# Performance work log

Measured on AMD Instinct MI355X. Metric: run time of the kernel, lower is better.

Reference implementation:

```python
import jax, jax.numpy as jnp
import numpy as np

B, S, H, NH, HD = 2, 2048, 1024, 16, 64
THETA = 10000.0


def setup_inputs() -> dict:
    key = jax.random.key(0)
    k1, k2, k3, k4, k5 = jax.random.split(key, 5)
    hidden_states = jax.random.normal(k1, (B, S, H), dtype=jnp.float32)
    # RoPE tables, interleaved-pair layout: [c0,c0,c1,c1,...] along head_dim
    inv_freq = 1.0 / (THETA ** (jnp.arange(0, HD, 2, dtype=jnp.float32) / HD))
    t = jnp.arange(S, dtype=jnp.float32)
    freqs = jnp.outer(t, inv_freq)                      # [S, HD//2]
    freqs_cos = jnp.repeat(jnp.cos(freqs), 2, axis=-1)  # [S, HD]
    freqs_sin = jnp.repeat(jnp.sin(freqs), 2, axis=-1)  # [S, HD]
    position_ids = jnp.arange(S, dtype=jnp.int32)
    w = 0.02
    Wq = jax.random.normal(k2, (H, H), dtype=jnp.float32) * w
    Wk = jax.random.normal(k3, (H, H), dtype=jnp.float32) * w
    Wv = jax.random.normal(k4, (H, H), dtype=jnp.float32) * w
    Wo = jax.random.normal(k5, (H, H), dtype=jnp.float32) * w
    return {"hidden_states": hidden_states, "freqs_cos": freqs_cos,
            "freqs_sin": freqs_sin, "position_ids": position_ids,
            "Wq": Wq, "Wk": Wk, "Wv": Wv, "Wo": Wo}


def _rotate_half_interleaved(x):
    # stack([-x[..., 1::2], x[..., ::2]], -1).reshape_as(x)
    xe = x.reshape(x.shape[:-1] + (HD // 2, 2))
    return jnp.stack([-xe[..., 1], xe[..., 0]], axis=-1).reshape(x.shape)


def reference(hidden_states, freqs_cos, freqs_sin, position_ids, Wq, Wk, Wv, Wo):
    b, s, _ = hidden_states.shape
    # QKV projections (torch Linear: y = x @ W.T), split into heads [b, nh, s, hd]
    q = jnp.einsum('bsh,oh->bso', hidden_states, Wq).reshape(b, s, NH, HD).transpose(0, 2, 1, 3)
    k = jnp.einsum('bsh,oh->bso', hidden_states, Wk).reshape(b, s, NH, HD).transpose(0, 2, 1, 3)
    v = jnp.einsum('bsh,oh->bso', hidden_states, Wv).reshape(b, s, NH, HD).transpose(0, 2, 1, 3)
    cos = freqs_cos[position_ids][None, None]  # [1, 1, s, hd]
    sin = freqs_sin[position_ids][None, None]
    rq = _rotate_half_interleaved(q)
    # NOTE: faithful to source bug — rotate_half_k is built from q, not k
    q = q * cos + rq * sin
    k = k * cos + rq * sin
    # causal SDPA, scale = 1/sqrt(head_dim)
    scores = jnp.einsum('bhqd,bhkd->bhqk', q, k) / jnp.sqrt(jnp.float32(HD))
    causal = jnp.tril(jnp.ones((s, s), dtype=bool))
    scores = jnp.where(causal, scores, jnp.float32(-1e30))
    attn = jax.nn.softmax(scores, axis=-1)
    out = jnp.einsum('bhqk,bhkd->bhqd', attn, v)
    out = out.transpose(0, 2, 1, 3).reshape(b, s, H)
    return jnp.einsum('bsh,oh->bso', out, Wo)
```

## Files before the change

kernel.cpp:

```cpp
#include <hip/hip_runtime.h>
#include <stdint.h>

#define BB 2
#define SS 2048
#define HH 1024
#define NHH 16
#define HDD 64

typedef short bf16s;
typedef __attribute__((ext_vector_type(8))) short short8;
typedef __attribute__((ext_vector_type(4))) short short4v;
typedef __attribute__((ext_vector_type(2))) short short2v;
typedef __attribute__((ext_vector_type(4))) float f32x4;
typedef _Float16 half4v __attribute__((ext_vector_type(4)));
typedef _Float16 half8v __attribute__((ext_vector_type(8)));
typedef __fp16 fp16x2 __attribute__((ext_vector_type(2)));

__device__ inline short f2bf(float f) {
  union { float f; uint32_t u; } v; v.f = f;
  uint32_t r = (v.u + 0x7fffu + ((v.u >> 16) & 1u)) >> 16;
  return (short)r;
}
__device__ inline float bf2f(short h) {
  union { uint32_t u; float f; } v; v.u = ((uint32_t)(uint16_t)h) << 16;
  return v.f;
}

__device__ __forceinline__ float exp2_raw(float x) {
  float r;
  asm("v_exp_f32 %0, %1\n\ts_nop 0" : "=v"(r) : "v"(x));
  return r;
}

__device__ inline void gld_lds16(const void* g, void* l) {
  __builtin_amdgcn_global_load_lds((const __attribute__((address_space(1))) void*)g,
                                   (__attribute__((address_space(3))) void*)l, 16, 0, 0);
}

__device__ inline void stv(short* C, size_t i, float v) { C[i] = f2bf(v); }
__device__ inline void stv(float* C, size_t i, float v) { C[i] = v; }

__device__ inline f32x4 mfma_k32(short8 a, short8 b, f32x4 c) {
  return __builtin_amdgcn_mfma_f32_16x16x32_bf16(a, b, c, 0, 0, 0);
}
__device__ inline f32x4 mfma_k32(half8v a, half8v b, f32x4 c) {
  return __builtin_amdgcn_mfma_f32_16x16x32_f16(a, b, c, 0, 0, 0);
}
template <typename ET> struct ftr;
template <> struct ftr<short>     { using v8 = short8; };
template <> struct ftr<_Float16>  { using v8 = half8v; };

__global__ __launch_bounds__(256) void convert_all(
    const float* __restrict__ x, const float* __restrict__ Wq,
    const float* __restrict__ Wk, const float* __restrict__ Wv,
    const float* __restrict__ Wo, bf16s* __restrict__ xb,
    bf16s* __restrict__ wqkv, _Float16* __restrict__ wof) {
  const long M1 = 1024L * 1024L;
  long e = (long)(blockIdx.x * blockDim.x + threadIdx.x) * 4;
  if (e < 7 * M1) {
    const float* src; bf16s* dst;
    if (e < 4 * M1)      { src = x  + e;            dst = xb   + e; }
    else if (e < 5 * M1) { src = Wq + (e - 4 * M1); dst = wqkv + (e - 4 * M1); }
    else if (e < 6 * M1) { src = Wk + (e - 5 * M1); dst = wqkv + (e - 4 * M1); }
    else                 { src = Wv + (e - 6 * M1); dst = wqkv + (e - 4 * M1); }
    float4 v = *(const float4*)src;
    short4v o;
    o.x = f2bf(v.x); o.y = f2bf(v.y); o.z = f2bf(v.z); o.w = f2bf(v.w);
    *(short4v*)dst = o;
  } else {
    float4 v = *(const float4*)(Wo + (e - 7 * M1));
    half4v o;
    o.x = (_Float16)v.x; o.y = (_Float16)v.y;
    o.z = (_Float16)v.z; o.w = (_Float16)v.w;
    *(half4v*)(wof + (e - 7 * M1)) = o;
  }
}

template <typename ET, typename OT, int MT>
__global__ __launch_bounds__(256) void gemm_bt(
    const ET* __restrict__ A, const ET* __restrict__ Bm,
    OT* __restrict__ C, int K, int ldc) {
  using V8 = typename ftr<ET>::v8;
  __shared__ __align__(16) ET As[MT * 32 * 64];
  __shared__ __align__(16) ET Bs[128 * 64];
  const int tid = threadIdx.x;
  const int lane = tid & 63, w = tid >> 6;
  const int quad = lane >> 4, mcol = lane & 15;
  const int bm = blockIdx.y * (MT * 32), bn = blockIdx.x * 128;
  const int wm = (w >> 1) * (MT * 16), wn = (w & 1) * 64;
  f32x4 acc[MT][4] = {};
  const int nkt = K >> 6;
  for (int kt = 0; kt < nkt; ++kt) {
    __syncthreads();
#pragma unroll
    for (int i = 0; i < MT; ++i) {
      int seg = (i * 4 + w) * 512;
      int flat = seg + lane * 8;
      int row = flat >> 6;
      int cpos = (flat >> 3) & 7;
      int cs = cpos ^ (row & 7);
      gld_lds16(A + (size_t)(bm + row) * K + kt * 64 + cs * 8, &As[seg]);
    }
#pragma unroll
    for (int i = 0; i < 4; ++i) {
      int seg = (i * 4 + w) * 512;
      int flat = seg + lane * 8;
      int row = flat >> 6;
      int cpos = (flat >> 3) & 7;
      int cs = cpos ^ (row & 7);
      gld_lds16(Bm + (size_t)(bn + row) * K + kt * 64 + cs * 8, &Bs[seg]);
    }
    __syncthreads();
#pragma unroll
    for (int ks = 0; ks < 2; ++ks) {
      V8 af[MT], bf[4];
#pragma unroll
      for (int mt = 0; mt < MT; ++mt) {
        int row = wm + mt * 16 + mcol;
        int cs = (ks * 4 + quad) ^ (row & 7);
        af[mt] = *(const V8*)&As[row * 64 + cs * 8];
      }
#pragma unroll
      for (int nt = 0; nt < 4; ++nt) {
        int row = wn + nt * 16 + mcol;
        int cs = (ks * 4 + quad) ^ (row & 7);
        bf[nt] = *(const V8*)&Bs[row * 64 + cs * 8];
      }
#pragma unroll
      for (int mt = 0; mt < MT; ++mt)
#pragma unroll
        for (int nt = 0; nt < 4; ++nt)
          acc[mt][nt] = mfma_k32(af[mt], bf[nt], acc[mt][nt]);
    }
  }
#pragma unroll
  for (int mt = 0; mt < MT; ++mt)
#pragma unroll
    for (int nt = 0; nt < 4; ++nt) {
      int r0 = bm + wm + mt * 16 + quad * 4;
      int c = bn + wn + nt * 16 + mcol;
#pragma unroll
      for (int r = 0; r < 4; ++r)
        stv(C, (size_t)(r0 + r) * ldc + c, acc[mt][nt][r]);
    }
}

__global__ __launch_bounds__(256) void postproc(
    const bf16s* __restrict__ qkv, const float* __restrict__ fcos,
    const float* __restrict__ fsin, const int* __restrict__ pos,
    bf16s* __restrict__ Q, bf16s* __restrict__ Kc, _Float16* __restrict__ Vt) {
  const float LOG2E = 1.4426950408889634f;
  const int st = blockIdx.x, bh = blockIdx.y;
  const int b = bh >> 4, h = bh & 15;
  const int tid = threadIdx.x;
  const int m0 = b * 2048 + st * 64;
  {
    const int row = tid >> 2, pc = tid & 3;
    const int s = st * 64 + row;
    const int p = pos[s];
    const bf16s* qp = qkv + (size_t)(m0 + row) * 3072 + h * 64 + pc * 16;
    short8 qv[2] = { *(const short8*)qp, *(const short8*)(qp + 8) };
    short8 kv[2] = { *(const short8*)(qp + 1024), *(const short8*)(qp + 1032) };
    const float* cp = fcos + (size_t)p * 64 + pc * 16;
    const float* sp = fsin + (size_t)p * 64 + pc * 16;
    short8 qo[2], ko[2];
#pragma unroll
    for (int hf = 0; hf < 2; ++hf)
#pragma unroll
      for (int j = 0; j < 4; ++j) {
        float c = cp[hf * 8 + 2 * j], sn = sp[hf * 8 + 2 * j];
        float q0 = bf2f(qv[hf][2 * j]), q1 = bf2f(qv[hf][2 * j + 1]);
        float k0 = bf2f(kv[hf][2 * j]), k1 = bf2f(kv[hf][2 * j + 1]);
        qo[hf][2 * j]     = f2bf((q0 * c - q1 * sn) * 0.125f);
        qo[hf][2 * j + 1] = f2bf((q1 * c + q0 * sn) * 0.125f);
        ko[hf][2 * j]     = f2bf((k0 * c - q1 * sn) * LOG2E);
        ko[hf][2 * j + 1] = f2bf((k1 * c + q0 * sn) * LOG2E);
      }
    size_t o = ((size_t)bh * 2048 + s) * 64 + pc * 16;
    *(short8*)&Q[o] = qo[0];  *(short8*)&Q[o + 8] = qo[1];
    *(short8*)&Kc[o] = ko[0]; *(short8*)&Kc[o + 8] = ko[1];
  }
  __shared__ __align__(16) _Float16 T[64 * 72];
#pragma unroll
  for (int p2 = 0; p2 < 2; ++p2) {
    int sl = p2 * 32 + (tid >> 3);
    int ch = tid & 7;
    short8 v = *(const short8*)&qkv[(size_t)(m0 + sl) * 3072 + 2048 + h * 64 + ch * 8];
#pragma unroll
    for (int j = 0; j < 8; ++j) T[(ch * 8 + j) * 72 + sl] = (_Float16)bf2f(v[j]);
  }
  __syncthreads();
#pragma unroll
  for (int p2 = 0; p2 < 2; ++p2) {
    int dl = p2 * 32 + (tid >> 3);
    int ch = tid & 7;
    half8v v = *(const half8v*)&T[dl * 72 + ch * 8];
    *(half8v*)&Vt[((size_t)bh * 64 + dl) * 2048 + st * 64 + ch * 8] = v;
  }
}

template <bool DOB>
__device__ __forceinline__ void step2(
    const bf16s* __restrict__ Ks, const _Float16* __restrict__ Vs,
    const short8* bqA, const short8* bqB,
    f32x4* OA, f32x4* OB, float& lA, float& lB,
    bool diagA, bool diagB, int w, int quad, int col) {
  f32x4 sA[4], sB[4];
#pragma unroll
  for (int t = 0; t < 4; ++t) {
    f32x4 a = {}, bb = {};
#pragma unroll
    for (int ks = 0; ks < 2; ++ks) {
      int krow = t * 16 + col;
      int cs = (ks * 4 + quad) ^ (krow & 7);
      short8 af = *(const short8*)&Ks[krow * 64 + cs * 8];
      a = __builtin_amdgcn_mfma_f32_16x16x32_bf16(af, bqA[ks], a, 0, 0, 0);
      if (DOB) bb = __builtin_amdgcn_mfma_f32_16x16x32_bf16(af, bqB[ks], bb, 0, 0, 0);
    }
    sA[t] = a;
    if (DOB) sB[t] = bb;
  }
  if (diagA) {
#pragma unroll
    for (int t = 0; t < 4; ++t)
#pragma unroll
      for (int r = 0; r < 4; ++r)
        if (t * 16 + quad * 4 + r > w * 16 + col) sA[t][r] = -1e30f;
  }
  if (DOB && diagB) {
#pragma unroll
    for (int t = 0; t < 4; ++t)
#pragma unroll
      for (int r = 0; r < 4; ++r)
        if (t * 16 + quad * 4 + r > w * 16 + col) sB[t][r] = -1e30f;
  }
  half4v paA[4], paB[4];
#pragma unroll
  for (int t = 0; t < 4; ++t) {
    {
      float p0 = exp2_raw(sA[t][0]), p1 = exp2_raw(sA[t][1]);
      float p2 = exp2_raw(sA[t][2]), p3 = exp2_raw(sA[t][3]);
      lA += (p0 + p1) + (p2 + p3);
      union { fp16x2 h2[2]; half4v h4; } u;
      u.h2[0] = __builtin_amdgcn_cvt_pkrtz(p0, p1);
      u.h2[1] = __builtin_amdgcn_cvt_pkrtz(p2, p3);
      paA[t] = u.h4;
    }
    if (DOB) {
      float p0 = exp2_raw(sB[t][0]), p1 = exp2_raw(sB[t][1]);
      float p2 = exp2_raw(sB[t][2]), p3 = exp2_raw(sB[t][3]);
      lB += (p0 + p1) + (p2 + p3);
      union { fp16x2 h2[2]; half4v h4; } u;
      u.h2[0] = __builtin_amdgcn_cvt_pkrtz(p0, p1);
      u.h2[1] = __builtin_amdgcn_cvt_pkrtz(p2, p3);
      paB[t] = u.h4;
    }
  }
#pragma unroll
  for (int t = 0; t < 4; ++t)
#pragma unroll
    for (int dt = 0; dt < 4; ++dt) {
      int vrow = dt * 16 + col;
      half4v bv = *(const half4v*)&Vs[vrow * 68 + t * 16 + quad * 4];
      OA[dt] = __builtin_amdgcn_mfma_f32_16x16x16f16(paA[t], bv, OA[dt], 0, 0, 0);
      if (DOB) OB[dt] = __builtin_amdgcn_mfma_f32_16x16x16f16(paB[t], bv, OB[dt], 0, 0, 0);
    }
}

__global__ __launch_bounds__(256) void attn(
    const bf16s* __restrict__ Q, const bf16s* __restrict__ Kb,
    const _Float16* __restrict__ Vt, _Float16* __restrict__ O) {
  __shared__ __align__(16) bf16s Ks[2][64 * 64];
  __shared__ __align__(16) _Float16 Vs[2][64 * 68];
  const int bh = blockIdx.y;
  const int tid = threadIdx.x, lane = tid & 63, w = tid >> 6;
  const int quad = lane >> 4, col = lane & 15;
  const size_t base = (size_t)bh * 2048 * 64;
  const _Float16* vbase = Vt + (size_t)bh * 64 * 2048;
  const int b = bh >> 4, h = bh & 15;
  const int x = blockIdx.x;
  const int qbA = 31 - x, qbB = x;

  short8 bqA[2], bqB[2];
  {
    const int qrA = qbA * 64 + w * 16 + col;
    const int qrB = qbB * 64 + w * 16 + col;
#pragma unroll
    for (int ks = 0; ks < 2; ++ks) {
      bqA[ks] = *(const short8*)&Q[base + (size_t)qrA * 64 + ks * 32 + quad * 8];
      bqB[ks] = *(const short8*)&Q[base + (size_t)qrB * 64 + ks * 32 + quad * 8];
    }
  }
  f32x4 OA[4] = {}, OB[4] = {};
  float lA = 0.f, lB = 0.f;

  const int vd = tid >> 2, vc = tid & 3;
  const _Float16* vsrc = vbase + (size_t)vd * 2048 + vc * 16;
  const int voff = vd * 68 + vc * 16;

  {
    half8v a0 = *(const half8v*)(vsrc);
    half8v a1 = *(const half8v*)(vsrc + 8);
    *(half8v*)&Vs[0][voff] = a0;
    *(half8v*)&Vs[0][voff + 8] = a1;
#pragma unroll
    for (int i = 0; i < 2; ++i) {
      int seg = (i * 4 + w) * 512;
      int flat = seg + lane * 8;
      int row = flat >> 6, cpos = (flat >> 3) & 7;
      int cs = cpos ^ (row & 7);
      gld_lds16(&Kb[base + (size_t)row * 64 + cs * 8], &Ks[0][seg]);
    }
  }

  for (int kt = 0; kt <= qbA; ++kt) {
    const int cur = kt & 1;
    __syncthreads();
    half8v n0, n1;
    const bool pf = (kt < qbA);
    if (pf) {
      n0 = *(const half8v*)(vsrc + (size_t)(kt + 1) * 64);
      n1 = *(const half8v*)(vsrc + (size_t)(kt + 1) * 64 + 8);
#pragma unroll
      for (int i = 0; i < 2; ++i) {
        int seg = (i * 4 + w) * 512;
        int flat = seg + lane * 8;
        int row = flat >> 6, cpos = (flat >> 3) & 7;
        int cs = cpos ^ (row & 7);
        gld_lds16(&Kb[base + (size_t)((kt + 1) * 64 + row) * 64 + cs * 8],
                  &Ks[cur ^ 1][seg]);
      }
    }
    if (kt <= qbB)
      step2<true>(Ks[cur], Vs[cur], bqA, bqB, OA, OB, lA, lB,
                  false, kt == qbB, w, quad, col);
    else
      step2<false>(Ks[cur], Vs[cur], bqA, bqB, OA, OB, lA, lB,
                   kt == qbA, false, w, quad, col);
    if (pf) {
      *(half8v*)&Vs[cur ^ 1][voff] = n0;
      *(half8v*)&Vs[cur ^ 1][voff + 8] = n1;
    }
  }

  lA += __shfl_xor(lA, 16); lA += __shfl_xor(lA, 32);
  lB += __shfl_xor(lB, 16); lB += __shfl_xor(lB, 32);

#pragma unroll
  for (int which = 0; which < 2; ++which) {
    const int qb = which ? qbB : qbA;
    const f32x4* Oacc = which ? OB : OA;
    const float l = which ? lB : lA;
    float l4[4];
#pragma unroll
    for (int r = 0; r < 4; ++r) l4[r] = __shfl(l, quad * 4 + r);
#pragma unroll
    for (int dt = 0; dt < 4; ++dt)
#pragma unroll
      for (int r = 0; r < 4; ++r) {
        int srow = qb * 64 + w * 16 + quad * 4 + r;
        O[((size_t)b * 2048 + srow) * 1024 + h * 64 + dt * 16 + col] =
            (_Float16)(Oacc[dt][r] / l4[r]);
      }
  }
}

extern "C" void kernel_launch(void* const* d_in, const int* in_sizes, int n_in,
                              void* d_out, int out_size, void* d_ws, size_t ws_size,
                              hipStream_t stream) {
  (void)in_sizes; (void)n_in; (void)out_size; (void)ws_size;
  const float* x  = (const float*)d_in[0];
  const float* fc = (const float*)d_in[1];
  const float* fs = (const float*)d_in[2];
  const int* pos  = (const int*)d_in[3];
  const float* Wq = (const float*)d_in[4];
  const float* Wk = (const float*)d_in[5];
  const float* Wv = (const float*)d_in[6];
  const float* Wo = (const float*)d_in[7];
  float* out = (float*)d_out;
  char* ws = (char*)d_ws;
  const size_t MB = 1024 * 1024;
  bf16s* xb    = (bf16s*)(ws);
  bf16s* wqkv  = (bf16s*)(ws + 8 * MB);
  _Float16* wof = (_Float16*)(ws + 14 * MB);
  bf16s* qkv   = (bf16s*)(ws + 16 * MB);
  bf16s* Qb    = (bf16s*)(ws + 40 * MB);
  bf16s* Kb    = (bf16s*)(ws + 48 * MB);
  _Float16* Vt = (_Float16*)(ws + 56 * MB);
  _Float16* Ob = (_Float16*)(ws);

  convert_all<<<8192, 256, 0, stream>>>(x, Wq, Wk, Wv, Wo, xb, wqkv, wof);
  gemm_bt<short, short, 4><<<dim3(24, 32), 256, 0, stream>>>(xb, wqkv, qkv, 1024, 3072);
  postproc<<<dim3(32, 32), 256, 0, stream>>>(qkv, fc, fs, pos, Qb, Kb, Vt);
  attn<<<dim3(16, 32), 256, 0, stream>>>(Qb, Kb, Vt, Ob);
  gemm_bt<_Float16, float, 2><<<dim3(8, 64), 256, 0, stream>>>(Ob, wof, out, 1024, 1024);
}
```

Baseline: 196.4 us.

## Split attention KV loop across two warp groups with LDS reduction

The attention kernel grows to 512 threads, and two groups of four warps each process alternating K/V tiles. Partial O and l accumulators are then combined through shared-memory scratch before the final store. This doubles the waves working per query block to raise occupancy and latency hiding. In exchange it drops the previous software prefetch double-buffering, since each iteration now loads and then syncs. It also adds reduction syncs and relies on the softmax not tracking a running max, which the existing step2 already assumes.

```diff
diff --git a/kernel.cpp b/kernel.cpp
--- a/kernel.cpp
+++ b/kernel.cpp
@@ -267,13 +267,16 @@
     }
 }
 
-__global__ __launch_bounds__(256) void attn(
+__global__ __launch_bounds__(512) void attn(
     const bf16s* __restrict__ Q, const bf16s* __restrict__ Kb,
     const _Float16* __restrict__ Vt, _Float16* __restrict__ O) {
   __shared__ __align__(16) bf16s Ks[2][64 * 64];
   __shared__ __align__(16) _Float16 Vs[2][64 * 68];
   const int bh = blockIdx.y;
-  const int tid = threadIdx.x, lane = tid & 63, w = tid >> 6;
+  const int tid = threadIdx.x, lane = tid & 63;
+  const int wid = tid >> 6;
+  const int grp = wid >> 2;
+  const int w = wid & 3;
   const int quad = lane >> 4, col = lane & 15;
   const size_t base = (size_t)bh * 2048 * 64;
   const _Float16* vbase = Vt + (size_t)bh * 64 * 2048;
@@ -294,74 +297,111 @@
   f32x4 OA[4] = {}, OB[4] = {};
   float lA = 0.f, lB = 0.f;
 
-  const int vd = tid >> 2, vc = tid & 3;
+  const int vtile = tid >> 8;
+  const int vr = tid & 255;
+  const int vd = vr >> 2, vc = vr & 3;
   const _Float16* vsrc = vbase + (size_t)vd * 2048 + vc * 16;
   const int voff = vd * 68 + vc * 16;
 
-  {
-    half8v a0 = *(const half8v*)(vsrc);
-    half8v a1 = *(const half8v*)(vsrc + 8);
-    *(half8v*)&Vs[0][voff] = a0;
-    *(half8v*)&Vs[0][voff + 8] = a1;
+  const int niters = (qbA + 2) >> 1;
+  for (int it = 0; it < niters; ++it) {
+    const int ks0 = 2 * it;
+    const int ks1g = 2 * it + 1;
+    const int ks1 = ks1g <= qbA ? ks1g : qbA;
+    const int myks = vtile ? ks1 : ks0;
+    half8v a0 = *(const half8v*)(vsrc + (size_t)myks * 64);
+    half8v a1 = *(const half8v*)(vsrc + (size_t)myks * 64 + 8);
+    __syncthreads();
+    *(half8v*)&Vs[vtile][voff] = a0;
+    *(half8v*)&Vs[vtile][voff + 8] = a1;
 #pragma unroll
     for (int i = 0; i < 2; ++i) {
-      int seg = (i * 4 + w) * 512;
+      int idx = i * 8 + wid;
+      int ktile = idx >> 3;
+      int seg = (idx & 7) * 512;
       int flat = seg + lane * 8;
       int row = flat >> 6, cpos = (flat >> 3) & 7;
       int cs = cpos ^ (row & 7);
-      gld_lds16(&Kb[base + (size_t)row * 64 + cs * 8], &Ks[0][seg]);
-    }
-  }
-
-  for (int kt = 0; kt <= qbA; ++kt) {
-    const int cur = kt & 1;
+      int src_kt = ktile ? ks1 : ks0;
+      gld_lds16(&Kb[base + (size_t)(src_kt * 64 + row) * 64 + cs * 8],
+                &Ks[ktile][seg]);
+    }
     __syncthreads();
-    half8v n0, n1;
-    const bool pf = (kt < qbA);
-    if (pf) {
-      n0 = *(const half8v*)(vsrc + (size_t)(kt + 1) * 64);
-      n1 = *(const half8v*)(vsrc + (size_t)(kt + 1) * 64 + 8);
-#pragma unroll
-      for (int i = 0; i < 2; ++i) {
-        int seg = (i * 4 + w) * 512;
-        int flat = seg + lane * 8;
-        int row = flat >> 6, cpos = (flat >> 3) & 7;
-        int cs = cpos ^ (row & 7);
-        gld_lds16(&Kb[base + (size_t)((kt + 1) * 64 + row) * 64 + cs * 8],
-                  &Ks[cur ^ 1][seg]);
-      }
-    }
-    if (kt <= qbB)
-      step2<true>(Ks[cur], Vs[cur], bqA, bqB, OA, OB, lA, lB,
-                  false, kt == qbB, w, quad, col);
-    else
-      step2<false>(Ks[cur], Vs[cur], bqA, bqB, OA, OB, lA, lB,
-                   kt == qbA, false, w, quad, col);
-    if (pf) {
-      *(half8v*)&Vs[cur ^ 1][voff] = n0;
-      *(half8v*)&Vs[cur ^ 1][voff + 8] = n1;
+    if (grp == 0) {
+      if (ks0 <= qbB)
+        step2<true>(Ks[0], Vs[0], bqA, bqB, OA, OB, lA, lB,
+                    ks0 == qbA, ks0 == qbB, w, quad, col);
+      else
+        step2<false>(Ks[0], Vs[0], bqA, bqB, OA, OB, lA, lB,
+                     ks0 == qbA, false, w, quad, col);
+    } else if (ks1g <= qbA) {
+      if (ks1g <= qbB)
+        step2<true>(Ks[1], Vs[1], bqA, bqB, OA, OB, lA, lB,
+                    ks1g == qbA, ks1g == qbB, w, quad, col);
+      else
+        step2<false>(Ks[1], Vs[1], bqA, bqB, OA, OB, lA, lB,
+                     ks1g == qbA, false, w, quad, col);
     }
   }
 
   lA += __shfl_xor(lA, 16); lA += __shfl_xor(lA, 32);
   lB += __shfl_xor(lB, 16); lB += __shfl_xor(lB, 32);
 
-#pragma unroll
-  for (int which = 0; which < 2; ++which) {
-    const int qb = which ? qbB : qbA;
-    const f32x4* Oacc = which ? OB : OA;
-    const float l = which ? lB : lA;
-    float l4[4];
-#pragma unroll
-    for (int r = 0; r < 4; ++r) l4[r] = __shfl(l, quad * 4 + r);
+  float* scrO = (float*)Ks;
+  float* scrL = (float*)Vs;
+  __syncthreads();
+  if (grp == 1) {
 #pragma unroll
     for (int dt = 0; dt < 4; ++dt)
 #pragma unroll
-      for (int r = 0; r < 4; ++r) {
-        int srow = qb * 64 + w * 16 + quad * 4 + r;
-        O[((size_t)b * 2048 + srow) * 1024 + h * 64 + dt * 16 + col] =
-            (_Float16)(Oacc[dt][r] / l4[r]);
-      }
+      for (int r = 0; r < 4; ++r)
+        scrO[(w * 64 + lane) * 16 + dt * 4 + r] = OA[dt][r];
+    scrL[w * 64 + lane] = lA;
+    scrL[256 + w * 64 + lane] = lB;
+  }
+  __syncthreads();
+  if (grp == 0) {
+#pragma unroll
+    for (int dt = 0; dt < 4; ++dt)
+#pragma unroll
+      for (int r = 0; r < 4; ++r)
+        OA[dt][r] += scrO[(w * 64 + lane) * 16 + dt * 4 + r];
+    lA += scrL[w * 64 + lane];
+    lB += scrL[256 + w * 64 + lane];
+  }
+  __syncthreads();
+  if (grp == 1) {
+#pragma unroll
+    for (int dt = 0; dt < 4; ++dt)
+#pragma unroll
+      for (int r = 0; r < 4; ++r)
+        scrO[(w * 64 + lane) * 16 + dt * 4 + r] = OB[dt][r];
+  }
+  __syncthreads();
+  if (grp == 0) {
+#pragma unroll
+    for (int dt = 0; dt < 4; ++dt)
+#pragma unroll
+      for (int r = 0; r < 4; ++r)
+        OB[dt][r] += scrO[(w * 64 + lane) * 16 + dt * 4 + r];
+
+#pragma unroll
+    for (int which = 0; which < 2; ++which) {
+      const int qb = which ? qbB : qbA;
+      const f32x4* Oacc = which ? OB : OA;
+      const float l = which ? lB : lA;
+      float l4[4];
+#pragma unroll
+      for (int r = 0; r < 4; ++r) l4[r] = __shfl(l, quad * 4 + r);
+#pragma unroll
+      for (int dt = 0; dt < 4; ++dt)
+#pragma unroll
+        for (int r = 0; r < 4; ++r) {
+          int srow = qb * 64 + w * 16 + quad * 4 + r;
+          O[((size_t)b * 2048 + srow) * 1024 + h * 64 + dt * 16 + col] =
+              (_Float16)(Oacc[dt][r] / l4[r]);
+        }
+    }
   }
 }
 
@@ -392,6 +432,6 @@
   convert_all<<<8192, 256, 0, stream>>>(x, Wq, Wk, Wv, Wo, xb, wqkv, wof);
   gemm_bt<short, short, 4><<<dim3(24, 32), 256, 0, stream>>>(xb, wqkv, qkv, 1024, 3072);
   postproc<<<dim3(32, 32), 256, 0, stream>>>(qkv, fc, fs, pos, Qb, Kb, Vt);
-  attn<<<dim3(16, 32), 256, 0, stream>>>(Qb, Kb, Vt, Ob);
+  attn<<<dim3(16, 32), 512, 0, stream>>>(Qb, Kb, Vt, Ob);
   gemm_bt<_Float16, float, 2><<<dim3(8, 64), 256, 0, stream>>>(Ob, wof, out, 1024, 1024);
 }
```

New measurement: 201.0 us. 1.02x slower.

## Fuse RoPE and V transpose into QKV GEMM epilogue; single-buffer attention tiles

Applied to the files above, without the earlier changes.

Replaces the QKV GEMM plus separate postproc kernel with one fused GEMM. Its column blocks are remapped so each tile holds matching Q and K head columns, letting the epilogue apply RoPE, scaling and the V transpose directly from registers. This removes the bf16 qkv intermediate round trip and one kernel launch. Separately, the attention kernel drops its double-buffered K/V prefetch for single-buffered loads with two barriers per tile. That cuts LDS use but exposes load latency. The fused epilogue also does scalar, scattered stores and per-element cos/sin loads.

```diff
diff --git a/kernel.cpp b/kernel.cpp
--- a/kernel.cpp
+++ b/kernel.cpp
@@ -10,7 +10,6 @@
 typedef short bf16s;
 typedef __attribute__((ext_vector_type(8))) short short8;
 typedef __attribute__((ext_vector_type(4))) short short4v;
-typedef __attribute__((ext_vector_type(2))) short short2v;
 typedef __attribute__((ext_vector_type(4))) float f32x4;
 typedef _Float16 half4v __attribute__((ext_vector_type(4)));
 typedef _Float16 half8v __attribute__((ext_vector_type(8)));
@@ -76,6 +75,111 @@
   }
 }
 
+__global__ __launch_bounds__(256) void gemm1_fused(
+    const bf16s* __restrict__ A, const bf16s* __restrict__ Bm,
+    const float* __restrict__ fcos, const float* __restrict__ fsin,
+    const int* __restrict__ pos, bf16s* __restrict__ Qb,
+    bf16s* __restrict__ Kb, _Float16* __restrict__ Vt) {
+  const float LOG2E = 1.4426950408889634f;
+  __shared__ __align__(16) bf16s As[128 * 64];
+  __shared__ __align__(16) bf16s Bs[128 * 64];
+  const int tid = threadIdx.x;
+  const int lane = tid & 63, w = tid >> 6;
+  const int quad = lane >> 4, mcol = lane & 15;
+  const int cb = blockIdx.x;
+  const bool isv = cb >= 16;
+  const int bm = blockIdx.y * 128;
+  const int wm = (w >> 1) * 64, wn = (w & 1) * 64;
+  f32x4 acc[4][4] = {};
+  for (int kt = 0; kt < 16; ++kt) {
+    __syncthreads();
+#pragma unroll
+    for (int i = 0; i < 4; ++i) {
+      int seg = (i * 4 + w) * 512;
+      int flat = seg + lane * 8;
+      int row = flat >> 6;
+      int cpos = (flat >> 3) & 7;
+      int cs = cpos ^ (row & 7);
+      gld_lds16(A + (size_t)(bm + row) * 1024 + kt * 64 + cs * 8, &As[seg]);
+      int grow;
+      if (isv) {
+        grow = 2048 + (cb - 16) * 128 + row;
+      } else {
+        int sub = row >> 5;
+        grow = (sub & 1) * 1024 + cb * 64 + (sub >> 1) * 32 + (row & 31);
+      }
+      gld_lds16(Bm + (size_t)grow * 1024 + kt * 64 + cs * 8, &Bs[seg]);
+    }
+    __syncthreads();
+#pragma unroll
+    for (int ks = 0; ks < 2; ++ks) {
+      short8 af[4], bf[4];
+#pragma unroll
+      for (int mt = 0; mt < 4; ++mt) {
+        int row = wm + mt * 16 + mcol;
+        int cs = (ks * 4 + quad) ^ (row & 7);
+        af[mt] = *(const short8*)&As[row * 64 + cs * 8];
+      }
+#pragma unroll
+      for (int nt = 0; nt < 4; ++nt) {
+        int row = wn + nt * 16 + mcol;
+        int cs = (ks * 4 + quad) ^ (row & 7);
+        bf[nt] = *(const short8*)&Bs[row * 64 + cs * 8];
+      }
+#pragma unroll
+      for (int mt = 0; mt < 4; ++mt)
+#pragma unroll
+        for (int nt = 0; nt < 4; ++nt)
+          acc[mt][nt] = __builtin_amdgcn_mfma_f32_16x16x32_bf16(af[mt], bf[nt], acc[mt][nt], 0, 0, 0);
+    }
+  }
+
+  if (!isv) {
+    const int h = cb;
+#pragma unroll
+    for (int mt = 0; mt < 4; ++mt) {
+      const int m0 = bm + wm + mt * 16 + quad * 4;
+#pragma unroll
+      for (int nt = 0; nt < 2; ++nt) {
+        const int d = (wn >> 1) + nt * 16 + mcol;
+#pragma unroll
+        for (int r = 0; r < 4; ++r) {
+          float qv = acc[mt][nt][r];
+          float kv = acc[mt][nt + 2][r];
+          float qp = __shfl_xor(qv, 1);
+          float rq = (d & 1) ? qp : -qp;
+          int m = m0 + r;
+          int bb = m >> 11, s = m & 2047;
+          int p = pos[s];
+          float c = fcos[p * 64 + d], sn = fsin[p * 64 + d];
+          size_t o = ((size_t)(bb * 16 + h) * 2048 + s) * 64 + d;
+          Qb[o] = f2bf((qv * c + rq * sn) * 0.125f);
+          Kb[o] = f2bf((kv * c + rq * sn) * LOG2E);
+        }
+      }
+    }
+  } else {
+    const int cv = cb - 16;
+#pragma unroll
+    for (int mt = 0; mt < 4; ++mt) {
+      const int m0 = bm + wm + mt * 16 + quad * 4;
+      const int bb = m0 >> 11, s0 = m0 & 2047;
+#pragma unroll
+      for (int nt = 0; nt < 4; ++nt) {
+        const int lc = wn + nt * 16;
+        const int hv = cv * 2 + (lc >> 6);
+        const int d = (lc & 63) + mcol;
+        half4v vv;
+        vv.x = (_Float16)acc[mt][nt][0];
+        vv.y = (_Float16)acc[mt][nt][1];
+        vv.z = (_Float16)acc[mt][nt][2];
+        vv.w = (_Float16)acc[mt][nt][3];
+        *(half4v*)&Vt[((size_t)(bb * 16 + hv) * 64 + d) * 2048 + s0] = vv;
+      }
+    }
+  }
+}
+
 template <typename ET, typename OT, int MT>
 __global__ __launch_bounds__(256) void gemm_bt(
     const ET* __restrict__ A, const ET* __restrict__ Bm,
@@ -145,60 +249,6 @@
     }
 }
 
-__global__ __launch_bounds__(256) void postproc(
-    const bf16s* __restrict__ qkv, const float* __restrict__ fcos,
-    const float* __restrict__ fsin, const int* __restrict__ pos,
-    bf16s* __restrict__ Q, bf16s* __restrict__ Kc, _Float16* __restrict__ Vt) {
-  const float LOG2E = 1.4426950408889634f;
-  const int st = blockIdx.x, bh = blockIdx.y;
-  const int b = bh >> 4, h = bh & 15;
-  const int tid = threadIdx.x;
-  const int m0 = b * 2048 + st * 64;
-  {
-    const int row = tid >> 2, pc = tid & 3;
-    const int s = st * 64 + row;
-    const int p = pos[s];
-    const bf16s* qp = qkv + (size_t)(m0 + row) * 3072 + h * 64 + pc * 16;
-    short8 qv[2] = { *(const short8*)qp, *(const short8*)(qp + 8) };
-    short8 kv[2] = { *(const short8*)(qp + 1024), *(const short8*)(qp + 1032) };
-    const float* cp = fcos + (size_t)p * 64 + pc * 16;
-    const float* sp = fsin + (size_t)p * 64 + pc * 16;
-    short8 qo[2], ko[2];
-#pragma unroll
-    for (int hf = 0; hf < 2; ++hf)
-#pragma unroll
-      for (int j = 0; j < 4; ++j) {
-        float c = cp[hf * 8 + 2 * j], sn = sp[hf * 8 + 2 * j];
-        float q0 = bf2f(qv[hf][2 * j]), q1 = bf2f(qv[hf][2 * j + 1]);
-        float k0 = bf2f(kv[hf][2 * j]), k1 = bf2f(kv[hf][2 * j + 1]);
-        qo[hf][2 * j]     = f2bf((q0 * c - q1 * sn) * 0.125f);
-        qo[hf][2 * j + 1] = f2bf((q1 * c + q0 * sn) * 0.125f);
-        ko[hf][2 * j]     = f2bf((k0 * c - q1 * sn) * LOG2E);
-        ko[hf][2 * j + 1] = f2bf((k1 * c + q0 * sn) * LOG2E);
-      }
-    size_t o = ((size_t)bh * 2048 + s) * 64 + pc * 16;
-    *(short8*)&Q[o] = qo[0];  *(short8*)&Q[o + 8] = qo[1];
-    *(short8*)&Kc[o] = ko[0]; *(short8*)&Kc[o + 8] = ko[1];
-  }
-  __shared__ __align__(16) _Float16 T[64 * 72];
-#pragma unroll
-  for (int p2 = 0; p2 < 2; ++p2) {
-    int sl = p2 * 32 + (tid >> 3);
-    int ch = tid & 7;
-    short8 v = *(const short8*)&qkv[(size_t)(m0 + sl) * 3072 + 2048 + h * 64 + ch * 8];
-#pragma unroll
-    for (int j = 0; j < 8; ++j) T[(ch * 8 + j) * 72 + sl] = (_Float16)bf2f(v[j]);
-  }
-  __syncthreads();
-#pragma unroll
-  for (int p2 = 0; p2 < 2; ++p2) {
-    int dl = p2 * 32 + (tid >> 3);
-    int ch = tid & 7;
-    half8v v = *(const half8v*)&T[dl * 72 + ch * 8];
-    *(half8v*)&Vt[((size_t)bh * 64 + dl) * 2048 + st * 64 + ch * 8] = v;
-  }
-}
-
 template <bool DOB>
 __device__ __forceinline__ void step2(
     const bf16s* __restrict__ Ks, const _Float16* __restrict__ Vs,
@@ -270,8 +320,8 @@
 __global__ __launch_bounds__(256) void attn(
     const bf16s* __restrict__ Q, const bf16s* __restrict__ Kb,
     const _Float16* __restrict__ Vt, _Float16* __restrict__ O) {
-  __shared__ __align__(16) bf16s Ks[2][64 * 64];
-  __shared__ __align__(16) _Float16 Vs[2][64 * 68];
+  __shared__ __align__(16) bf16s Ks[64 * 64];
+  __shared__ __align__(16) _Float16 Vs[64 * 68];
   const int bh = blockIdx.y;
   const int tid = threadIdx.x, lane = tid & 63, w = tid >> 6;
   const int quad = lane >> 4, col = lane & 15;
@@ -295,52 +345,27 @@
   float lA = 0.f, lB = 0.f;
 
   const int vd = tid >> 2, vc = tid & 3;
-  const _Float16* vsrc = vbase + (size_t)vd * 2048 + vc * 16;
-  const int voff = vd * 68 + vc * 16;
-
-  {
-    half8v a0 = *(const half8v*)(vsrc);
-    half8v a1 = *(const half8v*)(vsrc + 8);
-    *(half8v*)&Vs[0][voff] = a0;
-    *(half8v*)&Vs[0][voff + 8] = a1;
+  for (int kt = 0; kt <= qbA; ++kt) {
+    half8v vr0 = *(const half8v*)&vbase[(size_t)vd * 2048 + kt * 64 + vc * 16];
+    half8v vr1 = *(const half8v*)&vbase[(size_t)vd * 2048 + kt * 64 + vc * 16 + 8];
+    __syncthreads();
+    *(half8v*)&Vs[vd * 68 + vc * 16] = vr0;
+    *(half8v*)&Vs[vd * 68 + vc * 16 + 8] = vr1;
 #pragma unroll
     for (int i = 0; i < 2; ++i) {
       int seg = (i * 4 + w) * 512;
       int flat = seg + lane * 8;
       int row = flat >> 6, cpos = (flat >> 3) & 7;
       int cs = cpos ^ (row & 7);
-      gld_lds16(&Kb[base + (size_t)row * 64 + cs * 8], &Ks[0][seg]);
-    }
-  }
-
-  for (int kt = 0; kt <= qbA; ++kt) {
-    const int cur = kt & 1;
-    __syncthreads();
-    half8v n0, n1;
-    const bool pf = (kt < qbA);
-    if (pf) {
-      n0 = *(const half8v*)(vsrc + (size_t)(kt + 1) * 64);
-      n1 = *(const half8v*)(vsrc + (size_t)(kt + 1) * 64 + 8);
-#pragma unroll
-      for (int i = 0; i < 2; ++i) {
-        int seg = (i * 4 + w) * 512;
-        int flat = seg + lane * 8;
-        int row = flat >> 6, cpos = (flat >> 3) & 7;
-        int cs = cpos ^ (row & 7);
-        gld_lds16(&Kb[base + (size_t)((kt + 1) * 64 + row) * 64 + cs * 8],
-                  &Ks[cur ^ 1][seg]);
-      }
-    }
+      gld_lds16(&Kb[base + (size_t)(kt * 64 + row) * 64 + cs * 8], &Ks[seg]);
+    }
+    __syncthreads();
     if (kt <= qbB)
-      step2<true>(Ks[cur], Vs[cur], bqA, bqB, OA, OB, lA, lB,
+      step2<true>(Ks, Vs, bqA, bqB, OA, OB, lA, lB,
                   false, kt == qbB, w, quad, col);
     else
-      step2<false>(Ks[cur], Vs[cur], bqA, bqB, OA, OB, lA, lB,
+      step2<false>(Ks, Vs, bqA, bqB, OA, OB, lA, lB,
                    kt == qbA, false, w, quad, col);
-    if (pf) {
-      *(half8v*)&Vs[cur ^ 1][voff] = n0;
-      *(half8v*)&Vs[cur ^ 1][voff + 8] = n1;
-    }
   }
 
   lA += __shfl_xor(lA, 16); lA += __shfl_xor(lA, 32);
@@ -383,15 +408,13 @@
   bf16s* xb    = (bf16s*)(ws);
   bf16s* wqkv  = (bf16s*)(ws + 8 * MB);
   _Float16* wof = (_Float16*)(ws + 14 * MB);
-  bf16s* qkv   = (bf16s*)(ws + 16 * MB);
   bf16s* Qb    = (bf16s*)(ws + 40 * MB);
   bf16s* Kb    = (bf16s*)(ws + 48 * MB);
   _Float16* Vt = (_Float16*)(ws + 56 * MB);
   _Float16* Ob = (_Float16*)(ws);
 
   convert_all<<<8192, 256, 0, stream>>>(x, Wq, Wk, Wv, Wo, xb, wqkv, wof);
-  gemm_bt<short, short, 4><<<dim3(24, 32), 256, 0, stream>>>(xb, wqkv, qkv, 1024, 3072);
-  postproc<<<dim3(32, 32), 256, 0, stream>>>(qkv, fc, fs, pos, Qb, Kb, Vt);
+  gemm1_fused<<<dim3(24, 32), 256, 0, stream>>>(xb, wqkv, fc, fs, pos, Qb, Kb, Vt);
   attn<<<dim3(16, 32), 256, 0, stream>>>(Qb, Kb, Vt, Ob);
   gemm_bt<_Float16, float, 2><<<dim3(8, 64), 256, 0, stream>>>(Ob, wof, out, 1024, 1024);
 }
```

Measured after the change: 192.2 us. -2.2%, faster.
